# Performance work log

Hardware: AMD Instinct MI355X
Metric: run time of the kernel (lower is better)

## Reference

```python
import jax, jax.numpy as jnp
import numpy as np

RES = 14
KEY_DIM = 32
NUM_HEADS = 12
ATTN_RATIO = 4
DIM = 384
VAL_ATTN_DIM = ATTN_RATIO * KEY_DIM * NUM_HEADS  # 1536
QKV_DIM = VAL_ATTN_DIM + 2 * KEY_DIM * NUM_HEADS  # 2304
BN_EPS = 1e-5


def _bias_idxs():
    # torch.meshgrid default is 'ij'
    gy, gx = jnp.meshgrid(jnp.arange(RES), jnp.arange(RES), indexing='ij')
    pos = jnp.stack([gy.reshape(-1), gx.reshape(-1)])           # [2, N]
    rel = jnp.abs(pos[:, :, None] - pos[:, None, :])            # [2, N, N]
    return rel[0] * RES + rel[1]                                # [N, N] int


def _linear_bn(x, w, gamma, beta, mean, var):
    # bias-free Linear (torch weight layout [out,in]) + BatchNorm1d (eval)
    y = x @ w.T
    inv = gamma / jnp.sqrt(var + BN_EPS)
    return y * inv + (beta - mean * inv)


def setup_inputs() -> dict:
    key = jax.random.key(0)
    ks = jax.random.split(key, 12)
    B, N = 128, RES * RES
    f = jax.random.normal
    return {
        'x': f(ks[0], (B, N, DIM), jnp.float32),
        'qkv_w': f(ks[1], (QKV_DIM, DIM), jnp.float32) * 0.02,
        'qkv_gamma': f(ks[2], (QKV_DIM,), jnp.float32) * 0.1 + 1.0,
        'qkv_beta': f(ks[3], (QKV_DIM,), jnp.float32) * 0.1,
        'qkv_mean': f(ks[4], (QKV_DIM,), jnp.float32) * 0.1,
        'qkv_var': jax.random.uniform(ks[5], (QKV_DIM,), jnp.float32, 0.5, 1.5),
        'attn_biases': f(ks[6], (NUM_HEADS, RES * RES), jnp.float32) * 0.1,
        'proj_w': f(ks[7], (DIM, VAL_ATTN_DIM), jnp.float32) * 0.02,
        'proj_gamma': f(ks[8], (DIM,), jnp.float32) * 0.1 + 1.0,
        'proj_beta': f(ks[9], (DIM,), jnp.float32) * 0.1,
        'proj_mean': f(ks[10], (DIM,), jnp.float32) * 0.1,
        'proj_var': jax.random.uniform(ks[11], (DIM,), jnp.float32, 0.5, 1.5),
    }


def reference(x, qkv_w, qkv_gamma, qkv_beta, qkv_mean, qkv_var,
              attn_biases, proj_w, proj_gamma, proj_beta, proj_mean, proj_var):
    B, N, _ = x.shape
    scale = KEY_DIM ** -0.5
    qkv = _linear_bn(x, qkv_w, qkv_gamma, qkv_beta, qkv_mean, qkv_var)
    qkv = qkv.reshape(B, N, NUM_HEADS, -1)
    q = qkv[..., :KEY_DIM]                       # [B,N,H,dk]
    k = qkv[..., KEY_DIM:2 * KEY_DIM]            # [B,N,H,dk]
    v = qkv[..., 2 * KEY_DIM:]                   # [B,N,H,dv]
    bias = attn_biases[:, _bias_idxs()]          # [H,N,N]
    attn = jnp.einsum('bnhd,bmhd->bhnm', q, k) * scale + bias[None]
    attn = jax.nn.softmax(attn, axis=-1)
    out = jnp.einsum('bhnm,bmhd->bnhd', attn, v).reshape(B, N, VAL_ATTN_DIM)
    out = jax.nn.silu(out)
    return _linear_bn(out, proj_w, proj_gamma, proj_beta, proj_mean, proj_var)
```

## Files before the change

kernel.cpp:

```cpp
#include <hip/hip_runtime.h>
#include <cstdint>

#define NQ 196
#define DIMX 384
#define QKVD 2304
#define VAD 1536
#define NHD 12
#define MTOT 25088

#define KSTR 40
#define VSTR 232
#define TSTR 140

typedef unsigned int u32;
typedef unsigned short u16;
typedef __bf16 bf16_t;
typedef bf16_t bf16x8 __attribute__((ext_vector_type(8)));
typedef float f32x4 __attribute__((ext_vector_type(4)));

__device__ inline u16 f2b(float f) {
  u32 u = __float_as_uint(f);
  u32 r = (u + 0x7fffu + ((u >> 16) & 1u)) >> 16;
  return (u16)r;
}
__device__ inline float b2f(u16 u) { return __uint_as_float(((u32)u) << 16); }
__device__ inline int iabs(int v) { return v < 0 ? -v : v; }

__device__ inline void gld_lds16(const void* g, void* l) {
  __builtin_amdgcn_global_load_lds((__attribute__((address_space(1))) void*)g,
                                   (__attribute__((address_space(3))) void*)l,
                                   16, 0, 0);
}


__global__ void cvt_kernel(const float* __restrict__ in, u16* __restrict__ out, int n4) {
  int i = blockIdx.x * 256 + threadIdx.x;
  if (i >= n4) return;
  float4 v = ((const float4*)in)[i];
  ushort4 o;
  o.x = f2b(v.x); o.y = f2b(v.y); o.z = f2b(v.z); o.w = f2b(v.w);
  ((ushort4*)out)[i] = o;
}

__global__ void cvt_wqkv(const float* __restrict__ in, u16* __restrict__ out) {
  int i = blockIdx.x * 256 + threadIdx.x;
  if (i >= QKVD * DIMX / 4) return;
  const int newc = i / (DIMX / 4);
  const int kc = (i - newc * (DIMX / 4)) * 4;
  int oldc;
  if (newc < 384)      { int h = newc >> 5;              oldc = h * 192 + (newc & 31); }
  else if (newc < 768) { int t = newc - 384; int h = t >> 5; oldc = h * 192 + 32 + (t & 31); }
  else                 { int t = newc - 768; int h = t >> 7; oldc = h * 192 + 64 + (t & 127); }
  float4 v = *(const float4*)(in + (size_t)oldc * DIMX + kc);
  ushort4 o;
  o.x = f2b(v.x); o.y = f2b(v.y); o.z = f2b(v.z); o.w = f2b(v.w);
  *(ushort4*)(out + (size_t)newc * DIMX + kc) = o;
}

__global__ void bn_tab(const float* __restrict__ g, const float* __restrict__ be,
                       const float* __restrict__ mn, const float* __restrict__ vr,
                       float* __restrict__ inv, float* __restrict__ off, int n) {
  int i = blockIdx.x * 256 + threadIdx.x;
  if (i >= n) return;
  float iv = g[i] * rsqrtf(vr[i] + 1e-5f);
  inv[i] = iv;
  off[i] = be[i] - mn[i] * iv;
}

__global__ void bn_tab_qkv(const float* __restrict__ g, const float* __restrict__ be,
                           const float* __restrict__ mn, const float* __restrict__ vr,
                           float* __restrict__ inv, float* __restrict__ off) {
  int i = blockIdx.x * 256 + threadIdx.x;
  if (i >= QKVD) return;
  const int h = i / 192, r = i - h * 192;
  const int newc = (r < 32) ? h * 32 + r
                 : (r < 64) ? 384 + h * 32 + (r - 32)
                            : 768 + h * 128 + (r - 64);
  float iv = g[i] * rsqrtf(vr[i] + 1e-5f);
  inv[newc] = iv;
  off[newc] = be[i] - mn[i] * iv;
}


template <int MODE>
__global__ __launch_bounds__(256) void gemm_bt(
    const u16* __restrict__ A, const u16* __restrict__ B, int K,
    const float* __restrict__ inv, const float* __restrict__ off,
    u16* __restrict__ Qb, u16* __restrict__ Kb, u16* __restrict__ Vt,
    float* __restrict__ out) {
  constexpr int LDSU = (MODE == 0) ? 128 * TSTR : 8192;
  __shared__ __align__(16) u16 lds[LDSU];
  u16* As = lds;
  u16* Bs = lds + 4096;
  const int tid = threadIdx.x;
  const int wid = tid >> 6, lane = tid & 63;
  const int wm = wid & 1, wn = wid >> 1;
  const int fr = lane & 15, fk = (lane >> 4) << 3;
  const u16* Ab = A + (size_t)(blockIdx.y * 128) * K;
  const u16* Bb = B + (size_t)(blockIdx.x * 128) * K;
  const int c0 = (wid << 6) | lane;
  const int r0 = c0 >> 2, kc0 = (c0 & 3) << 3;
  const int c1 = c0 + 256;
  const int r1 = c1 >> 2, kc1 = (c1 & 3) << 3;

  f32x4 acc[4][4] = {};

  for (int k0 = 0; k0 < K; k0 += 32) {
    gld_lds16(Ab + (size_t)r0 * K + (k0 + kc0), &As[wid << 9]);
    gld_lds16(Ab + (size_t)r1 * K + (k0 + kc1), &As[2048 + (wid << 9)]);
    gld_lds16(Bb + (size_t)r0 * K + (k0 + kc0), &Bs[wid << 9]);
    gld_lds16(Bb + (size_t)r1 * K + (k0 + kc1), &Bs[2048 + (wid << 9)]);
    __syncthreads();
    bf16x8 av[4], bv[4];
#pragma unroll
    for (int t = 0; t < 4; t++)
      av[t] = *(const bf16x8*)&As[(wm * 64 + t * 16 + fr) * 32 + fk];
#pragma unroll
    for (int t = 0; t < 4; t++)
      bv[t] = *(const bf16x8*)&Bs[(wn * 64 + t * 16 + fr) * 32 + fk];
#pragma unroll
    for (int mt = 0; mt < 4; mt++)
#pragma unroll
      for (int nt = 0; nt < 4; nt++)
        acc[mt][nt] = __builtin_amdgcn_mfma_f32_16x16x32_bf16(av[mt], bv[nt], acc[mt][nt], 0, 0, 0);
    __syncthreads();
  }

  const int lrow0 = wm * 64 + ((lane >> 4) << 2);
  const int lcol0 = wn * 64 + fr;

  if (MODE == 0) {
    const int bx = blockIdx.x, by = blockIdx.y;
    const bool isV = bx >= 6;
#pragma unroll
    for (int nt = 0; nt < 4; nt++) {
      const int lc = lcol0 + nt * 16;
      const int gc = bx * 128 + lc;
      const float iv = inv[gc], of = off[gc];
#pragma unroll
      for (int mt = 0; mt < 4; mt++)
#pragma unroll
        for (int rg = 0; rg < 4; rg++) {
          const int lr = lrow0 + mt * 16 + rg;
          const u16 us = f2b(acc[mt][nt][rg] * iv + of);
          if (isV) lds[lc * TSTR + lr] = us;
          else     lds[lr * TSTR + lc] = us;
        }
    }
    __syncthreads();
    if (!isV) {
      u16* dstB = (bx < 3) ? Qb : Kb;
      const int h0 = (bx < 3 ? bx : bx - 3) * 4;
#pragma unroll
      for (int it = 0; it < 8; it++) {
        const int idx = it * 256 + tid;
        const int ch = idx & 3, hl = (idx >> 2) & 3, row = idx >> 4;
        const int rowg = by * 128 + row;
        const int b = rowg / 196, n = rowg - b * 196;
        const size_t bh = (size_t)(b * NHD + h0 + hl);
        const u16* src = &lds[row * TSTR + hl * 32 + ch * 8];
        uint2 a0 = *(const uint2*)src;
        uint2 a1 = *(const uint2*)(src + 4);
        *(uint4*)(dstB + (bh * NQ + n) * 32 + ch * 8) = make_uint4(a0.x, a0.y, a1.x, a1.y);
      }
    } else {
      const int h = bx - 6;
#pragma unroll
      for (int it = 0; it < 16; it++) {
        const int idx = it * 256 + tid;
        const int nk = idx & 31, col = idx >> 5;
        const int rowg = by * 128 + nk * 4;
        const int b = rowg / 196, n = rowg - b * 196;
        uint2 v = *(const uint2*)&lds[col * TSTR + nk * 4];
        *(uint2*)(Vt + ((size_t)(b * NHD + h) * 128 + col) * NQ + n) = v;
      }
    }
  } else {
    const int colb = blockIdx.x * 128 + lcol0;
    const int rowb = blockIdx.y * 128 + lrow0;
#pragma unroll
    for (int nt = 0; nt < 4; nt++) {
      const int col = colb + nt * 16;
      const float iv = inv[col], of = off[col];
#pragma unroll
      for (int mt = 0; mt < 4; mt++)
#pragma unroll
        for (int rg = 0; rg < 4; rg++) {
          const int row = rowb + mt * 16 + rg;
          out[(size_t)row * DIMX + col] = acc[mt][nt][rg] * iv + of;
        }
    }
  }
}


__global__ __launch_bounds__(512) void attn_kernel(
    const u16* __restrict__ Qg, const u16* __restrict__ Kg,
    const u16* __restrict__ Vtg, const float* __restrict__ biases,
    u16* __restrict__ AO) {
  __shared__ __align__(16) u16 Ks[208 * KSTR];
  __shared__ __align__(16) u16 Vs[128 * VSTR];
  __shared__ __align__(16) u16 Ps[8][16 * VSTR];
  __shared__ __align__(16) float biasS[NQ];

  const int tid = threadIdx.x, wid = tid >> 6, lane = tid & 63;
  const int fr = lane & 15, fj = lane >> 4, fk = fj << 3;
  const int bh = blockIdx.x, b = bh / NHD, h = bh - b * NHD;
  const float scale = 0.17677669529663687f;

  for (int i = tid; i < NQ * 4; i += 512) {
    const int m = i >> 2, kc = (i & 3) << 3;
    uint4 v = *(const uint4*)(Kg + ((size_t)bh * NQ + m) * 32 + kc);
    *(uint4*)&Ks[m * KSTR + kc] = v;
  }
  {
    const u32* src = (const u32*)(Vtg + (size_t)bh * 128 * NQ);
    u32* dst = (u32*)Vs;
    for (int i = tid; i < 128 * 98; i += 512) {
      const int d = i / 98, nc = i - d * 98;
      dst[d * (VSTR / 2) + nc] = src[i];
    }
    for (int i = tid; i < 128 * 18; i += 512) {
      const int d = i / 18, nc = 98 + (i - d * 18);
      dst[d * (VSTR / 2) + nc] = 0u;
    }
  }
  if (tid < NQ) biasS[tid] = biases[h * NQ + tid];
  {
    const int row = lane >> 2, c = 208 + (lane & 3) * 4;
    *(uint2*)&Ps[wid][row * VSTR + c] = make_uint2(0u, 0u);
  }
  __syncthreads();

  for (int rt = wid; rt < 13; rt += 8) {
    int qrow = rt * 16 + fr; qrow = qrow > 195 ? 195 : qrow;
    const bf16x8 qf = *(const bf16x8*)(Qg + ((size_t)bh * NQ + qrow) * 32 + fk);

    f32x4 s[13];
#pragma unroll
    for (int t = 0; t < 13; t++) {
      const bf16x8 kf = *(const bf16x8*)&Ks[(t * 16 + fr) * KSTR + fk];
      f32x4 z = {0.f, 0.f, 0.f, 0.f};
      s[t] = __builtin_amdgcn_mfma_f32_16x16x32_bf16(qf, kf, z, 0, 0, 0);
    }

    int yn[4], xn[4];
#pragma unroll
    for (int rg = 0; rg < 4; rg++) {
      int n = rt * 16 + fj * 4 + rg;
      int y = (n * 586) >> 13; y = y > 13 ? 13 : y;
      yn[rg] = y; xn[rg] = n - y * 14;
    }
#pragma unroll
    for (int t = 0; t < 13; t++) {
      const int m = t * 16 + fr;
      const bool valid = m < NQ;
      int ym = (m * 586) >> 13; ym = ym > 13 ? 13 : ym;
      const int xm = m - ym * 14;
#pragma unroll
      for (int rg = 0; rg < 4; rg++) {
        int idx = iabs(yn[rg] - ym) * 14 + iabs(xn[rg] - xm);
        idx = idx > 195 ? 195 : idx;
        const float bv = biasS[idx];
        s[t][rg] = valid ? (s[t][rg] * scale + bv) : -1e30f;
      }
    }
    float rinv[4];
#pragma unroll
    for (int rg = 0; rg < 4; rg++) {
      float mx = s[0][rg];
#pragma unroll
      for (int t = 1; t < 13; t++) mx = fmaxf(mx, s[t][rg]);
      mx = fmaxf(mx, __shfl_xor(mx, 1));
      mx = fmaxf(mx, __shfl_xor(mx, 2));
      mx = fmaxf(mx, __shfl_xor(mx, 4));
      mx = fmaxf(mx, __shfl_xor(mx, 8));
      float ls = 0.f;
#pragma unroll
      for (int t = 0; t < 13; t++) {
        const float e = __expf(s[t][rg] - mx);
        s[t][rg] = e;
        ls += e;
      }
      ls += __shfl_xor(ls, 1);
      ls += __shfl_xor(ls, 2);
      ls += __shfl_xor(ls, 4);
      ls += __shfl_xor(ls, 8);
      rinv[rg] = 1.f / ls;
    }
#pragma unroll
    for (int t = 0; t < 13; t++)
#pragma unroll
      for (int rg = 0; rg < 4; rg++)
        Ps[wid][(fj * 4 + rg) * VSTR + t * 16 + fr] = f2b(s[t][rg]);
    __threadfence_block();

    f32x4 o[8] = {};
#pragma unroll
    for (int kc = 0; kc < 7; kc++) {
      const bf16x8 pf = *(const bf16x8*)&Ps[wid][fr * VSTR + kc * 32 + fk];
#pragma unroll
      for (int dt = 0; dt < 8; dt++) {
        const bf16x8 vf = *(const bf16x8*)&Vs[(dt * 16 + fr) * VSTR + kc * 32 + fk];
        o[dt] = __builtin_amdgcn_mfma_f32_16x16x32_bf16(pf, vf, o[dt], 0, 0, 0);
      }
    }
#pragma unroll
    for (int rg = 0; rg < 4; rg++) {
      const int n = rt * 16 + fj * 4 + rg;
      if (n < NQ) {
        const float rv = rinv[rg];
#pragma unroll
        for (int dt = 0; dt < 8; dt++) {
          float x = o[dt][rg] * rv;
          x = x / (1.f + __expf(-x));
          AO[((size_t)(b * NQ + n)) * VAD + h * 128 + dt * 16 + fr] = f2b(x);
        }
      }
    }
    __threadfence_block();
  }
}


extern "C" void kernel_launch(void* const* d_in, const int* in_sizes, int n_in,
                              void* d_out, int out_size, void* d_ws, size_t ws_size,
                              hipStream_t stream) {
  const float* x          = (const float*)d_in[0];
  const float* qkv_w      = (const float*)d_in[1];
  const float* qkv_gamma  = (const float*)d_in[2];
  const float* qkv_beta   = (const float*)d_in[3];
  const float* qkv_mean   = (const float*)d_in[4];
  const float* qkv_var    = (const float*)d_in[5];
  const float* attn_bias  = (const float*)d_in[6];
  const float* proj_w     = (const float*)d_in[7];
  const float* proj_gamma = (const float*)d_in[8];
  const float* proj_beta  = (const float*)d_in[9];
  const float* proj_mean  = (const float*)d_in[10];
  const float* proj_var   = (const float*)d_in[11];

  const size_t szXB    = (size_t)MTOT * DIMX * 2;
  const size_t szQKVW  = (size_t)QKVD * DIMX * 2;
  const size_t szPROJW = (size_t)DIMX * VAD * 2;
  const size_t szQK    = (size_t)128 * NHD * NQ * 32 * 2;
  const size_t szV     = (size_t)128 * NHD * 128 * NQ * 2;
  const size_t szAO    = (size_t)MTOT * VAD * 2;
  const size_t szX     = (szXB + szQKVW > szAO) ? (szXB + szQKVW) : szAO;

  char* w = (char*)d_ws;
  u16* projwb = (u16*)w; w += szPROJW;
  float* inv1 = (float*)w; w += QKVD * 4;
  float* off1 = (float*)w; w += QKVD * 4;
  float* inv2 = (float*)w; w += DIMX * 4;
  float* off2 = (float*)w; w += DIMX * 4;
  u16* Qb = (u16*)w; w += szQK;
  u16* Kb = (u16*)w; w += szQK;
  u16* Vt = (u16*)w; w += szV;
  char* regionX = w; w += szX;
  u16* xb    = (u16*)regionX;
  u16* qkvwb = (u16*)(regionX + szXB);
  u16* AO    = (u16*)regionX;

  if ((size_t)(w - (char*)d_ws) > ws_size) return;

  cvt_kernel<<<MTOT * DIMX / 4 / 256, 256, 0, stream>>>(x, xb, MTOT * DIMX / 4);
  cvt_wqkv<<<(QKVD * DIMX / 4 + 255) / 256, 256, 0, stream>>>(qkv_w, qkvwb);
  cvt_kernel<<<DIMX * VAD / 4 / 256, 256, 0, stream>>>(proj_w, projwb, DIMX * VAD / 4);
  bn_tab_qkv<<<(QKVD + 255) / 256, 256, 0, stream>>>(qkv_gamma, qkv_beta, qkv_mean, qkv_var, inv1, off1);
  bn_tab<<<(DIMX + 255) / 256, 256, 0, stream>>>(proj_gamma, proj_beta, proj_mean, proj_var, inv2, off2, DIMX);

  gemm_bt<0><<<dim3(QKVD / 128, MTOT / 128), 256, 0, stream>>>(
      xb, qkvwb, DIMX, inv1, off1, Qb, Kb, Vt, nullptr);
  attn_kernel<<<128 * NHD, 512, 0, stream>>>(Qb, Kb, Vt, attn_bias, AO);
  gemm_bt<1><<<dim3(DIMX / 128, MTOT / 128), 256, 0, stream>>>(
      AO, projwb, VAD, inv2, off2, nullptr, nullptr, nullptr, (float*)d_out);
}
```

Measured before the change: 401.6 us.

## Precompute MFMA-layout bias tiles, stage attention output through LDS, row-wise V copy

Adds a small pre-kernel that expands the relative-position bias into per-head tiles laid out in MFMA fragment order, with padding masks included. The attention kernel can then load these tiles directly instead of computing per-element indices and gathering from LDS. Attention output is written to LDS first and stored to global as 16-byte rows instead of scattered 2-byte writes. The V staging loop is also rewritten as per-row copies to avoid integer divides. The cost is an extra launch, about 2 MB of workspace, and reads of the bias table from global/L2.

```diff
diff --git a/kernel.cpp b/kernel.cpp
--- a/kernel.cpp
+++ b/kernel.cpp
@@ -79,6 +79,27 @@
   float iv = g[i] * rsqrtf(vr[i] + 1e-5f);
   inv[newc] = iv;
   off[newc] = be[i] - mn[i] * iv;
+}
+
+__global__ void bias_tiles(const float* __restrict__ biases, float* __restrict__ bt) {
+  const int blk = blockIdx.x;
+  const int h = blk / 169, r2 = blk - h * 169;
+  const int rt = r2 / 13, t = r2 - rt * 13;
+  const int lane = threadIdx.x;
+  const int fr = lane & 15, fj = lane >> 4;
+  const int m = t * 16 + fr;
+  const bool mv = m < NQ;
+  const int ym = mv ? m / 14 : 0;
+  const int xm = mv ? (m - ym * 14) : 0;
+  f32x4 v;
+#pragma unroll
+  for (int rg = 0; rg < 4; rg++) {
+    int n = rt * 16 + fj * 4 + rg;
+    n = n > 195 ? 195 : n;
+    const int yn = n / 14, xn = n - yn * 14;
+    v[rg] = mv ? biases[h * NQ + iabs(yn - ym) * 14 + iabs(xn - xm)] : -1e30f;
+  }
+  *((f32x4*)bt + (size_t)blk * 64 + lane) = v;
 }
 
 
@@ -196,12 +217,11 @@
 
 __global__ __launch_bounds__(512) void attn_kernel(
     const u16* __restrict__ Qg, const u16* __restrict__ Kg,
-    const u16* __restrict__ Vtg, const float* __restrict__ biases,
+    const u16* __restrict__ Vtg, const float* __restrict__ biasT,
     u16* __restrict__ AO) {
   __shared__ __align__(16) u16 Ks[208 * KSTR];
   __shared__ __align__(16) u16 Vs[128 * VSTR];
   __shared__ __align__(16) u16 Ps[8][16 * VSTR];
-  __shared__ __align__(16) float biasS[NQ];
 
   const int tid = threadIdx.x, wid = tid >> 6, lane = tid & 63;
   const int fr = lane & 15, fj = lane >> 4, fk = fj << 3;
@@ -213,19 +233,19 @@
     uint4 v = *(const uint4*)(Kg + ((size_t)bh * NQ + m) * 32 + kc);
     *(uint4*)&Ks[m * KSTR + kc] = v;
   }
+  if (tid < 240) ((u32*)Ks)[3920 + tid] = 0u;
   {
     const u32* src = (const u32*)(Vtg + (size_t)bh * 128 * NQ);
     u32* dst = (u32*)Vs;
-    for (int i = tid; i < 128 * 98; i += 512) {
-      const int d = i / 98, nc = i - d * 98;
-      dst[d * (VSTR / 2) + nc] = src[i];
-    }
-    for (int i = tid; i < 128 * 18; i += 512) {
-      const int d = i / 18, nc = 98 + (i - d * 18);
-      dst[d * (VSTR / 2) + nc] = 0u;
-    }
-  }
-  if (tid < NQ) biasS[tid] = biases[h * NQ + tid];
+    const int c1 = lane + 64;
+    const int rEnd = wid * 16 + 16;
+    for (int r = wid * 16; r < rEnd; r++) {
+      const u32* srow = src + r * 98;
+      u32* drow = dst + r * (VSTR / 2);
+      drow[lane] = srow[lane];
+      if (c1 < VSTR / 2) drow[c1] = (c1 < 98) ? srow[c1] : 0u;
+    }
+  }
   {
     const int row = lane >> 2, c = 208 + (lane & 3) * 4;
     *(uint2*)&Ps[wid][row * VSTR + c] = make_uint2(0u, 0u);
@@ -244,27 +264,16 @@
       s[t] = __builtin_amdgcn_mfma_f32_16x16x32_bf16(qf, kf, z, 0, 0, 0);
     }
 
-    int yn[4], xn[4];
-#pragma unroll
-    for (int rg = 0; rg < 4; rg++) {
-      int n = rt * 16 + fj * 4 + rg;
-      int y = (n * 586) >> 13; y = y > 13 ? 13 : y;
-      yn[rg] = y; xn[rg] = n - y * 14;
-    }
-#pragma unroll
-    for (int t = 0; t < 13; t++) {
-      const int m = t * 16 + fr;
-      const bool valid = m < NQ;
-      int ym = (m * 586) >> 13; ym = ym > 13 ? 13 : ym;
-      const int xm = m - ym * 14;
-#pragma unroll
-      for (int rg = 0; rg < 4; rg++) {
-        int idx = iabs(yn[rg] - ym) * 14 + iabs(xn[rg] - xm);
-        idx = idx > 195 ? 195 : idx;
-        const float bv = biasS[idx];
-        s[t][rg] = valid ? (s[t][rg] * scale + bv) : -1e30f;
-      }
-    }
+    const f32x4* btp = (const f32x4*)biasT + ((size_t)(h * 169 + rt * 13) * 64 + lane);
+    f32x4 bt[13];
+#pragma unroll
+    for (int t = 0; t < 13; t++) bt[t] = btp[t * 64];
+#pragma unroll
+    for (int t = 0; t < 13; t++)
+#pragma unroll
+      for (int rg = 0; rg < 4; rg++)
+        s[t][rg] = s[t][rg] * scale + bt[t][rg];
+
     float rinv[4];
 #pragma unroll
     for (int rg = 0; rg < 4; rg++) {
@@ -307,15 +316,23 @@
     }
 #pragma unroll
     for (int rg = 0; rg < 4; rg++) {
-      const int n = rt * 16 + fj * 4 + rg;
+      const float rv = rinv[rg];
+#pragma unroll
+      for (int dt = 0; dt < 8; dt++) {
+        float x = o[dt][rg] * rv;
+        x = x / (1.f + __expf(-x));
+        Ps[wid][(fj * 4 + rg) * VSTR + dt * 16 + fr] = f2b(x);
+      }
+    }
+    __threadfence_block();
+#pragma unroll
+    for (int it = 0; it < 4; it++) {
+      const int idx = it * 64 + lane;
+      const int row = idx >> 4, dc = idx & 15;
+      const int n = rt * 16 + row;
       if (n < NQ) {
-        const float rv = rinv[rg];
-#pragma unroll
-        for (int dt = 0; dt < 8; dt++) {
-          float x = o[dt][rg] * rv;
-          x = x / (1.f + __expf(-x));
-          AO[((size_t)(b * NQ + n)) * VAD + h * 128 + dt * 16 + fr] = f2b(x);
-        }
+        uint4 v = *(const uint4*)&Ps[wid][row * VSTR + dc * 8];
+        *(uint4*)(AO + ((size_t)(b * NQ + n)) * VAD + h * 128 + dc * 8) = v;
       }
     }
     __threadfence_block();
@@ -345,6 +362,7 @@
   const size_t szQK    = (size_t)128 * NHD * NQ * 32 * 2;
   const size_t szV     = (size_t)128 * NHD * 128 * NQ * 2;
   const size_t szAO    = (size_t)MTOT * VAD * 2;
+  const size_t szBT    = (size_t)NHD * 169 * 64 * 4 * 4;
   const size_t szX     = (szXB + szQKVW > szAO) ? (szXB + szQKVW) : szAO;
 
   char* w = (char*)d_ws;
@@ -353,6 +371,7 @@
   float* off1 = (float*)w; w += QKVD * 4;
   float* inv2 = (float*)w; w += DIMX * 4;
   float* off2 = (float*)w; w += DIMX * 4;
+  float* biasT = (float*)w; w += szBT;
   u16* Qb = (u16*)w; w += szQK;
   u16* Kb = (u16*)w; w += szQK;
   u16* Vt = (u16*)w; w += szV;
@@ -368,10 +387,11 @@
   cvt_kernel<<<DIMX * VAD / 4 / 256, 256, 0, stream>>>(proj_w, projwb, DIMX * VAD / 4);
   bn_tab_qkv<<<(QKVD + 255) / 256, 256, 0, stream>>>(qkv_gamma, qkv_beta, qkv_mean, qkv_var, inv1, off1);
   bn_tab<<<(DIMX + 255) / 256, 256, 0, stream>>>(proj_gamma, proj_beta, proj_mean, proj_var, inv2, off2, DIMX);
+  bias_tiles<<<NHD * 169, 64, 0, stream>>>(attn_bias, biasT);
 
   gemm_bt<0><<<dim3(QKVD / 128, MTOT / 128), 256, 0, stream>>>(
       xb, qkvwb, DIMX, inv1, off1, Qb, Kb, Vt, nullptr);
-  attn_kernel<<<128 * NHD, 512, 0, stream>>>(Qb, Kb, Vt, attn_bias, AO);
+  attn_kernel<<<128 * NHD, 512, 0, stream>>>(Qb, Kb, Vt, biasT, AO);
   gemm_bt<1><<<dim3(DIMX / 128, MTOT / 128), 256, 0, stream>>>(
       AO, projwb, VAD, inv2, off2, nullptr, nullptr, nullptr, (float*)d_out);
 }
```

After: 429.3 us. 1.07x slower.
